# Kernel optimization log

Measured on AMD Instinct MI355X. Metric: run time of the kernel, lower is better.

The kernel has to match this reference:

```python
import jax, jax.numpy as jnp
import numpy as np
from jax import lax

B, D, BOND, OUT = 16384, 784, 5, 10

def setup_inputs() -> dict:
    key = jax.random.key(0)
    k = jax.random.split(key, 6)
    x = jax.random.uniform(k[0], (B, D), dtype=jnp.float32)
    core_first = jax.random.normal(k[1], (1, 2, BOND), dtype=jnp.float32) * 0.1
    cores_mid = jax.random.normal(k[2], (D - 2, BOND, 2, BOND), dtype=jnp.float32) * 0.1
    core_last = jax.random.normal(k[3], (BOND, 2, 1), dtype=jnp.float32) * 0.1
    # xavier_uniform for fc.weight with fan_in=1, fan_out=OUT
    bound = float(np.sqrt(6.0 / (1 + OUT)))
    fc_w = jax.random.uniform(k[4], (OUT, 1), dtype=jnp.float32, minval=-bound, maxval=bound)
    fc_b = jnp.zeros((OUT,), dtype=jnp.float32)
    return {"x": x, "core_first": core_first, "cores_mid": cores_mid,
            "core_last": core_last, "fc_w": fc_w, "fc_b": fc_b}

def reference(x, core_first, cores_mid, core_last, fc_w, fc_b):
    # x: [B, D] -> feature map [B, D, 2] = stack(1-x, x)
    xs = jnp.stack([1.0 - x, x], axis=-1)            # [B, D, 2]
    # first core: (1, 2, bond) -> initial carry [B, bond]
    carry0 = jnp.einsum('bi,ir->br', xs[:, 0], core_first[0])  # [B, bond]
    # sequential tensor-train contraction over middle sites via scan
    xs_mid = jnp.moveaxis(xs[:, 1:-1], 1, 0)          # [D-2, B, 2]
    def step(carry, inp):
        xi, core = inp                                # xi: [B,2], core: [bond,2,bond]
        carry = jnp.einsum('bl,bi,lir->br', carry, xi, core)
        return carry, None
    carry, _ = lax.scan(step, carry0, (xs_mid, cores_mid))
    # last core: (bond, 2, 1) -> scalar per batch element
    vlast = jnp.einsum('bi,li->bl', xs[:, -1], core_last[:, :, 0])  # [B, bond]
    res = jnp.sum(carry * vlast, axis=-1, keepdims=True)            # [B, 1]
    out = res @ fc_w.T + fc_b                          # [B, OUT]
    return out
```

## Files before the change

kernel.cpp:

```cpp
#include <hip/hip_runtime.h>


typedef float v4f __attribute__((ext_vector_type(4)));
typedef float v2f __attribute__((ext_vector_type(2)));

constexpr int Bn     = 16384;
constexpr int Dn     = 784;
constexpr int NOUT   = 10;
constexpr int NPAIR  = 390;
constexpr int PVEC   = 20;
constexpr int PMAT   = 25;
constexpr int RHP0   = 195;
constexpr int BWD_P0 = 370;
constexpr int PAIR_F = 100;
constexpr int WROFF  = Bn * 5;

__device__ __forceinline__ v4f splat4(float x) { v4f v = {x, x, x, x}; return v; }
__device__ __forceinline__ v4f fma4(v4f a, v4f b, v4f c) {
    return __builtin_elementwise_fma(a, b, c);
}

struct Frag { v4f r[5]; float c4[5]; };
struct CMat { v4f row[5]; v4f c4v; float c44; };

__device__ __forceinline__ void build_C(CMat& C, const float* __restrict__ s,
                                        v2f xc) {
    const float xa = xc[0], xb = xc[1], xab = xa * xb;
    const v4f va = splat4(xa), vb = splat4(xb), vp = splat4(xab);
    const v4f* s4 = (const v4f*)s;
#pragma unroll
    for (int l = 0; l < 5; ++l)
        C.row[l] = fma4(vp, s4[15 + l], fma4(vb, s4[10 + l], fma4(va, s4[5 + l], s4[l])));
#pragma unroll
    for (int l = 0; l < 4; ++l) {
        v4f cq = s4[20 + l];
        C.c4v[l] = fmaf(xab, cq[3], fmaf(xb, cq[2], fmaf(xa, cq[1], cq[0])));
    }
    {
        v4f cq = s4[24];
        C.c44 = fmaf(xab, cq[3], fmaf(xb, cq[2], fmaf(xa, cq[1], cq[0])));
    }
}

__device__ __forceinline__ void matmulIP(Frag& M, const CMat& C) {
#pragma unroll
    for (int i = 0; i < 5; ++i) {
        v4f acc  = splat4(M.r[i][0]) * C.row[0];
        float a4 = M.r[i][0] * C.c4v[0];
#pragma unroll
        for (int l = 1; l < 4; ++l) {
            acc = fma4(splat4(M.r[i][l]), C.row[l], acc);
            a4  = fmaf(M.r[i][l], C.c4v[l], a4);
        }
        acc = fma4(splat4(M.c4[i]), C.row[4], acc);
        a4  = fmaf(M.c4[i], C.c44, a4);
        M.r[i] = acc; M.c4[i] = a4;
    }
}

__device__ __forceinline__ void vecstepC(v4f& cv, float& c4, const CMat& C) {
    v4f acc  = splat4(cv[0]) * C.row[0];
    float a4 = cv[0] * C.c4v[0];
#pragma unroll
    for (int l = 1; l < 4; ++l) {
        acc = fma4(splat4(cv[l]), C.row[l], acc);
        a4  = fmaf(cv[l], C.c4v[l], a4);
    }
    acc = fma4(splat4(c4), C.row[4], acc);
    a4  = fmaf(c4, C.c44, a4);
    cv = acc; c4 = a4;
}

__global__ void prepack_pairs(const float* __restrict__ cm, float* __restrict__ pk)
{
    int idx = blockIdx.x * 256 + threadIdx.x;
    if (idx >= NPAIR * 100) return;
    int p = idx / 100, rest = idx - p * 100;
    int q = rest / 25, e = rest - q * 25;
    int l = e / 5, r = e - l * 5;
    int m1 = 2 * p + 1, m2 = 2 * p + 2;
    const float* L = cm + (size_t)(m1 * 5 + l) * 10;
    float acc = 0.f;
#pragma unroll
    for (int k = 0; k < 5; ++k) {
        float Lk = (q & 1) ? (L[5 + k] - L[k]) : L[k];
        const float* R = cm + (size_t)(m2 * 5 + k) * 10;
        float Rk = (q & 2) ? (R[5 + r] - R[r]) : R[r];
        acc = fmaf(Lk, Rk, acc);
    }
    int wl = l, wr = r;
    if (p >= BWD_P0) { wl = r; wr = l; }
    int off;
    if (wr < 4)      off = q * 20 + wl * 4 + wr;
    else if (wl < 4) off = 80 + wl * 4 + q;
    else             off = 96 + q;
    pk[(size_t)p * PAIR_F + off] = acc;
}

__global__ __launch_bounds__(512, 2)
void mps_half_kernel(const float* __restrict__ x,
                     const float* __restrict__ core_first,
                     const float* __restrict__ cores_mid,
                     const float* __restrict__ core_last,
                     const float* __restrict__ pk,
                     float* __restrict__ out)
{
    __shared__ float matbuf[4][25][128];

    const int lane = threadIdx.x & 63;
    const int wave = threadIdx.x >> 6;
    const int wu   = __builtin_amdgcn_readfirstlane(wave);
    const int g    = blockIdx.x >> 1;
    const int h    = blockIdx.x & 1;
    const int rowA = g * 128 + lane;
    const int rowB = rowA + 64;
    const v2f* __restrict__ xA2 = (const v2f*)(x + (size_t)rowA * Dn);
    const v2f* __restrict__ xB2 = (const v2f*)(x + (size_t)rowB * Dn);

    if (wu >= 1) {
        const int p0 = (h == 0 ? PVEC : RHP0) + PMAT * (wu - 1);

        Frag MA, MB;
        MA.r[0] = {1,0,0,0}; MA.r[1] = {0,1,0,0}; MA.r[2] = {0,0,1,0};
        MA.r[3] = {0,0,0,1}; MA.r[4] = {0,0,0,0};
        MA.c4[0] = 0; MA.c4[1] = 0; MA.c4[2] = 0; MA.c4[3] = 0; MA.c4[4] = 1;
        MB = MA;

        v2f xA = xA2[p0 + 1], xB = xB2[p0 + 1];
#pragma unroll 1
        for (int j = 0; j < PMAT; ++j) {
            const float* s = pk + (size_t)(p0 + j) * PAIR_F;
            v2f nxA = xA2[p0 + j + 2], nxB = xB2[p0 + j + 2];
            CMat C;
            build_C(C, s, xA);  matmulIP(MA, C);
            build_C(C, s, xB);  matmulIP(MB, C);
            xA = nxA; xB = nxB;
        }

        const int ord  = (h == 0) ? (wu - 1) : (7 - wu);
        const bool ph1 = (ord < 4);
        const int  k   = ph1 ? ord : ord - 4;
        if (ph1) {
#pragma unroll
            for (int i = 0; i < 5; ++i) {
#pragma unroll
                for (int r = 0; r < 4; ++r) {
                    matbuf[k][i * 5 + r][lane]      = MA.r[i][r];
                    matbuf[k][i * 5 + r][lane + 64] = MB.r[i][r];
                }
                matbuf[k][i * 5 + 4][lane]      = MA.c4[i];
                matbuf[k][i * 5 + 4][lane + 64] = MB.c4[i];
            }
        }
        __syncthreads();
        __syncthreads();
        if (!ph1) {
#pragma unroll
            for (int i = 0; i < 5; ++i) {
#pragma unroll
                for (int r = 0; r < 4; ++r) {
                    matbuf[k][i * 5 + r][lane]      = MA.r[i][r];
                    matbuf[k][i * 5 + r][lane + 64] = MB.r[i][r];
                }
                matbuf[k][i * 5 + 4][lane]      = MA.c4[i];
                matbuf[k][i * 5 + 4][lane + 64] = MB.c4[i];
            }
        }
        __syncthreads();
    } else if (h == 0) {
        v2f xA01 = xA2[0], xB01 = xB2[0];
        float clA[5], clB[5], cnA[5], cnB[5];
#pragma unroll
        for (int r = 0; r < 5; ++r) {
            float d = core_first[5 + r] - core_first[r];
            clA[r] = fmaf(xA01[0], d, core_first[r]);
            clB[r] = fmaf(xB01[0], d, core_first[r]);
        }
        const float* cm0 = cores_mid;
#pragma unroll
        for (int r = 0; r < 5; ++r) {
            float aA = 0.f, aB = 0.f;
#pragma unroll
            for (int l = 0; l < 5; ++l) {
                float base = cm0[l * 10 + r], d = cm0[l * 10 + 5 + r] - base;
                aA = fmaf(clA[l], fmaf(xA01[1], d, base), aA);
                aB = fmaf(clB[l], fmaf(xB01[1], d, base), aB);
            }
            cnA[r] = aA; cnB[r] = aB;
        }
        v4f cvA = {cnA[0], cnA[1], cnA[2], cnA[3]};
        v4f cvB = {cnB[0], cnB[1], cnB[2], cnB[3]};
        float c4A = cnA[4], c4B = cnB[4];

        v2f xA = xA2[1], xB = xB2[1];
#pragma unroll 1
        for (int p = 0; p < PVEC; ++p) {
            const float* s = pk + (size_t)p * PAIR_F;
            v2f nxA = xA2[p + 2], nxB = xB2[p + 2];
            CMat C;
            build_C(C, s, xA);  vecstepC(cvA, c4A, C);
            build_C(C, s, xB);  vecstepC(cvB, c4B, C);
            xA = nxA; xB = nxB;
        }
        clA[0] = cvA[0]; clA[1] = cvA[1]; clA[2] = cvA[2]; clA[3] = cvA[3]; clA[4] = c4A;
        clB[0] = cvB[0]; clB[1] = cvB[1]; clB[2] = cvB[2]; clB[3] = cvB[3]; clB[4] = c4B;

        __syncthreads();
#pragma unroll 1
        for (int k = 0; k < 4; ++k) {
            float vA[5], vB[5];
#pragma unroll
            for (int r = 0; r < 5; ++r) {
                vA[r] = clA[0] * matbuf[k][r][lane];
                vB[r] = clB[0] * matbuf[k][r][lane + 64];
            }
#pragma unroll
            for (int l = 1; l < 5; ++l)
#pragma unroll
                for (int r = 0; r < 5; ++r) {
                    vA[r] = fmaf(clA[l], matbuf[k][l * 5 + r][lane],      vA[r]);
                    vB[r] = fmaf(clB[l], matbuf[k][l * 5 + r][lane + 64], vB[r]);
                }
#pragma unroll
            for (int r = 0; r < 5; ++r) { clA[r] = vA[r]; clB[r] = vB[r]; }
        }
        __syncthreads();
        __syncthreads();
#pragma unroll 1
        for (int k = 0; k < 3; ++k) {
            float vA[5], vB[5];
#pragma unroll
            for (int r = 0; r < 5; ++r) {
                vA[r] = clA[0] * matbuf[k][r][lane];
                vB[r] = clB[0] * matbuf[k][r][lane + 64];
            }
#pragma unroll
            for (int l = 1; l < 5; ++l)
#pragma unroll
                for (int r = 0; r < 5; ++r) {
                    vA[r] = fmaf(clA[l], matbuf[k][l * 5 + r][lane],      vA[r]);
                    vB[r] = fmaf(clB[l], matbuf[k][l * 5 + r][lane + 64], vB[r]);
                }
#pragma unroll
            for (int r = 0; r < 5; ++r) { clA[r] = vA[r]; clB[r] = vB[r]; }
        }
        float* oA = out + (size_t)rowA * 5;
        float* oB = out + (size_t)rowB * 5;
#pragma unroll
        for (int i = 0; i < 5; ++i) { oA[i] = clA[i]; oB[i] = clB[i]; }
    } else {
        v2f xAz = xA2[391], xBz = xB2[391];
        float vlA[5], vlB[5], vnA[5], vnB[5];
#pragma unroll
        for (int l = 0; l < 5; ++l) {
            float base = core_last[2 * l], d = core_last[2 * l + 1] - base;
            vlA[l] = fmaf(xAz[1], d, base);
            vlB[l] = fmaf(xBz[1], d, base);
        }
        const float* cmL = cores_mid + (size_t)781 * 50;
#pragma unroll
        for (int l = 0; l < 5; ++l) {
            float aA = 0.f, aB = 0.f;
#pragma unroll
            for (int r = 0; r < 5; ++r) {
                float base = cmL[l * 10 + r], d = cmL[l * 10 + 5 + r] - base;
                aA = fmaf(fmaf(xAz[0], d, base), vlA[r], aA);
                aB = fmaf(fmaf(xBz[0], d, base), vlB[r], aB);
            }
            vnA[l] = aA; vnB[l] = aB;
        }
        v4f cvA = {vnA[0], vnA[1], vnA[2], vnA[3]};
        v4f cvB = {vnB[0], vnB[1], vnB[2], vnB[3]};
        float c4A = vnA[4], c4B = vnB[4];

        v2f xA = xA2[390], xB = xB2[390];
#pragma unroll 1
        for (int p = 389; p >= BWD_P0; --p) {
            const float* s = pk + (size_t)p * PAIR_F;
            v2f nxA = xA2[p], nxB = xB2[p];
            CMat C;
            build_C(C, s, xA);  vecstepC(cvA, c4A, C);
            build_C(C, s, xB);  vecstepC(cvB, c4B, C);
            xA = nxA; xB = nxB;
        }
        float uA[5] = {cvA[0], cvA[1], cvA[2], cvA[3], c4A};
        float uB[5] = {cvB[0], cvB[1], cvB[2], cvB[3], c4B};

        __syncthreads();
#pragma unroll 1
        for (int k = 0; k < 4; ++k) {
            float vA[5], vB[5];
#pragma unroll
            for (int i = 0; i < 5; ++i) {
                float aA = matbuf[k][i * 5][lane]      * uA[0];
                float aB = matbuf[k][i * 5][lane + 64] * uB[0];
#pragma unroll
                for (int l = 1; l < 5; ++l) {
                    aA = fmaf(matbuf[k][i * 5 + l][lane],      uA[l], aA);
                    aB = fmaf(matbuf[k][i * 5 + l][lane + 64], uB[l], aB);
                }
                vA[i] = aA; vB[i] = aB;
            }
#pragma unroll
            for (int i = 0; i < 5; ++i) { uA[i] = vA[i]; uB[i] = vB[i]; }
        }
        __syncthreads();
        __syncthreads();
#pragma unroll 1
        for (int k = 0; k < 3; ++k) {
            float vA[5], vB[5];
#pragma unroll
            for (int i = 0; i < 5; ++i) {
                float aA = matbuf[k][i * 5][lane]      * uA[0];
                float aB = matbuf[k][i * 5][lane + 64] * uB[0];
#pragma unroll
                for (int l = 1; l < 5; ++l) {
                    aA = fmaf(matbuf[k][i * 5 + l][lane],      uA[l], aA);
                    aB = fmaf(matbuf[k][i * 5 + l][lane + 64], uB[l], aB);
                }
                vA[i] = aA; vB[i] = aB;
            }
#pragma unroll
            for (int i = 0; i < 5; ++i) { uA[i] = vA[i]; uB[i] = vB[i]; }
        }
        float* oA = out + WROFF + (size_t)rowA * 5;
        float* oB = out + WROFF + (size_t)rowB * 5;
#pragma unroll
        for (int i = 0; i < 5; ++i) { oA[i] = uA[i]; oB[i] = uB[i]; }
    }
}

__global__ __launch_bounds__(256)
void finish_dot(const float* __restrict__ outF, float* __restrict__ res)
{
    int r = blockIdx.x * 256 + threadIdx.x;
    const float* vl = outF + (size_t)r * 5;
    const float* wr = outF + WROFF + (size_t)r * 5;
    float s = vl[0] * wr[0];
#pragma unroll
    for (int i = 1; i < 5; ++i) s = fmaf(vl[i], wr[i], s);
    res[r] = s;
}

__global__ __launch_bounds__(256)
void finish_out(const float* __restrict__ res, const float* __restrict__ fc_w,
                const float* __restrict__ fc_b, float* __restrict__ out)
{
    int r = blockIdx.x * 256 + threadIdx.x;
    float rv = res[r];
    float* o = out + (size_t)r * NOUT;
#pragma unroll
    for (int j = 0; j < NOUT; ++j) o[j] = fmaf(rv, fc_w[j], fc_b[j]);
}

extern "C" void kernel_launch(void* const* d_in, const int* in_sizes, int n_in,
                              void* d_out, int out_size, void* d_ws, size_t ws_size,
                              hipStream_t stream) {
    const float* x          = (const float*)d_in[0];
    const float* core_first = (const float*)d_in[1];
    const float* cores_mid  = (const float*)d_in[2];
    const float* core_last  = (const float*)d_in[3];
    const float* fc_w       = (const float*)d_in[4];
    const float* fc_b       = (const float*)d_in[5];
    float* out              = (float*)d_out;
    float* pk               = (float*)d_ws;
    float* res              = (float*)d_ws;

    hipLaunchKernelGGL(prepack_pairs, dim3((NPAIR * 100 + 255) / 256), dim3(256),
                       0, stream, cores_mid, pk);
    hipLaunchKernelGGL(mps_half_kernel, dim3(256), dim3(512), 0, stream,
                       x, core_first, cores_mid, core_last, pk, out);
    hipLaunchKernelGGL(finish_dot, dim3(Bn / 256), dim3(256), 0, stream,
                       out, res);
    hipLaunchKernelGGL(finish_out, dim3(Bn / 256), dim3(256), 0, stream,
                       res, fc_w, fc_b, out);
}
```

Measured before the change: 146.0 us.

## Split the chain into four segments per row group across 512 blocks

Adds a quarter-split kernel in which each 128-row group is handled by four blocks instead of two. Each block covers a shorter stretch of sites: the two middle segments fold their partial 5x5 transfer matrices and write them to workspace, and a new finish kernel combines them with the left and right vectors. This doubles the block count and shortens the per-wave sequential chains to expose more parallelism on the GPU. In exchange it adds global traffic for the intermediate matrices and an extra combine step. The old half-split path remains as a fallback when the workspace is too small.

```diff
diff --git a/kernel.cpp b/kernel.cpp
--- a/kernel.cpp
+++ b/kernel.cpp
@@ -8,12 +8,10 @@
 constexpr int Dn     = 784;
 constexpr int NOUT   = 10;
 constexpr int NPAIR  = 390;
-constexpr int PVEC   = 20;
-constexpr int PMAT   = 25;
-constexpr int RHP0   = 195;
-constexpr int BWD_P0 = 370;
 constexpr int PAIR_F = 100;
 constexpr int WROFF  = Bn * 5;
+constexpr int PK_F   = 40960;
+constexpr int M_OFF  = PK_F;
 
 __device__ __forceinline__ v4f splat4(float x) { v4f v = {x, x, x, x}; return v; }
 __device__ __forceinline__ v4f fma4(v4f a, v4f b, v4f c) {
@@ -71,7 +69,40 @@
     cv = acc; c4 = a4;
 }
 
-__global__ void prepack_pairs(const float* __restrict__ cm, float* __restrict__ pk)
+__device__ __forceinline__ void mat_chain(Frag& MA, Frag& MB, int p0, int n,
+                                          const float* __restrict__ pk,
+                                          const v2f* __restrict__ xA2,
+                                          const v2f* __restrict__ xB2) {
+    v2f xA = xA2[p0 + 1], xB = xB2[p0 + 1];
+#pragma unroll 1
+    for (int j = 0; j < n; ++j) {
+        const float* s = pk + (size_t)(p0 + j) * PAIR_F;
+        v2f nxA = xA2[p0 + j + 2], nxB = xB2[p0 + j + 2];
+        CMat C;
+        build_C(C, s, xA);  matmulIP(MA, C);
+        build_C(C, s, xB);  matmulIP(MB, C);
+        xA = nxA; xB = nxB;
+    }
+}
+
+__device__ __forceinline__ void foldM(Frag& M, const float (*mb)[128], int ln) {
+#pragma unroll
+    for (int i = 0; i < 5; ++i) {
+        float v[5];
+#pragma unroll
+        for (int r = 0; r < 5; ++r) {
+            float a = M.r[i][0] * mb[r][ln];
+#pragma unroll
+            for (int l = 1; l < 4; ++l) a = fmaf(M.r[i][l], mb[l * 5 + r][ln], a);
+            a = fmaf(M.c4[i], mb[20 + r][ln], a);
+            v[r] = a;
+        }
+        M.r[i] = {v[0], v[1], v[2], v[3]}; M.c4[i] = v[4];
+    }
+}
+
+__global__ void prepack_pairs(const float* __restrict__ cm, float* __restrict__ pk,
+                              int bwd0)
 {
     int idx = blockIdx.x * 256 + threadIdx.x;
     if (idx >= NPAIR * 100) return;
@@ -89,13 +120,306 @@
         acc = fmaf(Lk, Rk, acc);
     }
     int wl = l, wr = r;
-    if (p >= BWD_P0) { wl = r; wr = l; }
+    if (p >= bwd0) { wl = r; wr = l; }
     int off;
     if (wr < 4)      off = q * 20 + wl * 4 + wr;
     else if (wl < 4) off = 80 + wl * 4 + q;
     else             off = 96 + q;
     pk[(size_t)p * PAIR_F + off] = acc;
 }
+
+
+__global__ __launch_bounds__(512, 2)
+void mps_quarter_kernel(const float* __restrict__ x,
+                        const float* __restrict__ core_first,
+                        const float* __restrict__ cores_mid,
+                        const float* __restrict__ core_last,
+                        float* __restrict__ ws,
+                        float* __restrict__ out)
+{
+    __shared__ float matbuf[4][25][128];
+
+    const float* __restrict__ pk = ws;
+    const int lane = threadIdx.x & 63;
+    const int wave = threadIdx.x >> 6;
+    const int wu   = __builtin_amdgcn_readfirstlane(wave);
+    const int g    = blockIdx.x >> 2;
+    const int seg  = blockIdx.x & 3;
+    const int rowA = g * 128 + lane;
+    const int rowB = rowA + 64;
+    const v2f* __restrict__ xA2 = (const v2f*)(x + (size_t)rowA * Dn);
+    const v2f* __restrict__ xB2 = (const v2f*)(x + (size_t)rowB * Dn);
+
+    if (wu >= 1) {
+        const int m0 = (seg == 0) ? 13 : (seg == 1) ? 111 : (seg == 2) ? 209 : 293;
+        const int p0 = m0 + 12 * (wu - 1);
+
+        Frag MA, MB;
+        MA.r[0] = {1,0,0,0}; MA.r[1] = {0,1,0,0}; MA.r[2] = {0,0,1,0};
+        MA.r[3] = {0,0,0,1}; MA.r[4] = {0,0,0,0};
+        MA.c4[0] = 0; MA.c4[1] = 0; MA.c4[2] = 0; MA.c4[3] = 0; MA.c4[4] = 1;
+        MB = MA;
+
+        mat_chain(MA, MB, p0, 12, pk, xA2, xB2);
+
+        const int ord  = (seg == 3) ? (7 - wu) : (wu - 1);
+        const bool ph1 = (ord < 4);
+        const int  k   = ph1 ? ord : ord - 4;
+        if (ph1) {
+#pragma unroll
+            for (int i = 0; i < 5; ++i) {
+#pragma unroll
+                for (int r = 0; r < 4; ++r) {
+                    matbuf[k][i * 5 + r][lane]      = MA.r[i][r];
+                    matbuf[k][i * 5 + r][lane + 64] = MB.r[i][r];
+                }
+                matbuf[k][i * 5 + 4][lane]      = MA.c4[i];
+                matbuf[k][i * 5 + 4][lane + 64] = MB.c4[i];
+            }
+        }
+        __syncthreads();
+        __syncthreads();
+        if (!ph1) {
+#pragma unroll
+            for (int i = 0; i < 5; ++i) {
+#pragma unroll
+                for (int r = 0; r < 4; ++r) {
+                    matbuf[k][i * 5 + r][lane]      = MA.r[i][r];
+                    matbuf[k][i * 5 + r][lane + 64] = MB.r[i][r];
+                }
+                matbuf[k][i * 5 + 4][lane]      = MA.c4[i];
+                matbuf[k][i * 5 + 4][lane + 64] = MB.c4[i];
+            }
+        }
+        __syncthreads();
+    } else if (seg == 0) {
+        v2f xA01 = xA2[0], xB01 = xB2[0];
+        float clA[5], clB[5], cnA[5], cnB[5];
+#pragma unroll
+        for (int r = 0; r < 5; ++r) {
+            float d = core_first[5 + r] - core_first[r];
+            clA[r] = fmaf(xA01[0], d, core_first[r]);
+            clB[r] = fmaf(xB01[0], d, core_first[r]);
+        }
+        const float* cm0 = cores_mid;
+#pragma unroll
+        for (int r = 0; r < 5; ++r) {
+            float aA = 0.f, aB = 0.f;
+#pragma unroll
+            for (int l = 0; l < 5; ++l) {
+                float base = cm0[l * 10 + r], d = cm0[l * 10 + 5 + r] - base;
+                aA = fmaf(clA[l], fmaf(xA01[1], d, base), aA);
+                aB = fmaf(clB[l], fmaf(xB01[1], d, base), aB);
+            }
+            cnA[r] = aA; cnB[r] = aB;
+        }
+        v4f cvA = {cnA[0], cnA[1], cnA[2], cnA[3]};
+        v4f cvB = {cnB[0], cnB[1], cnB[2], cnB[3]};
+        float c4A = cnA[4], c4B = cnB[4];
+
+        v2f xA = xA2[1], xB = xB2[1];
+#pragma unroll 1
+        for (int p = 0; p < 13; ++p) {
+            const float* s = pk + (size_t)p * PAIR_F;
+            v2f nxA = xA2[p + 2], nxB = xB2[p + 2];
+            CMat C;
+            build_C(C, s, xA);  vecstepC(cvA, c4A, C);
+            build_C(C, s, xB);  vecstepC(cvB, c4B, C);
+            xA = nxA; xB = nxB;
+        }
+        clA[0] = cvA[0]; clA[1] = cvA[1]; clA[2] = cvA[2]; clA[3] = cvA[3]; clA[4] = c4A;
+        clB[0] = cvB[0]; clB[1] = cvB[1]; clB[2] = cvB[2]; clB[3] = cvB[3]; clB[4] = c4B;
+
+        __syncthreads();
+#pragma unroll 1
+        for (int k = 0; k < 4; ++k) {
+            float vA[5], vB[5];
+#pragma unroll
+            for (int r = 0; r < 5; ++r) {
+                vA[r] = clA[0] * matbuf[k][r][lane];
+                vB[r] = clB[0] * matbuf[k][r][lane + 64];
+            }
+#pragma unroll
+            for (int l = 1; l < 5; ++l)
+#pragma unroll
+                for (int r = 0; r < 5; ++r) {
+                    vA[r] = fmaf(clA[l], matbuf[k][l * 5 + r][lane],      vA[r]);
+                    vB[r] = fmaf(clB[l], matbuf[k][l * 5 + r][lane + 64], vB[r]);
+                }
+#pragma unroll
+            for (int r = 0; r < 5; ++r) { clA[r] = vA[r]; clB[r] = vB[r]; }
+        }
+        __syncthreads();
+        __syncthreads();
+#pragma unroll 1
+        for (int k = 0; k < 3; ++k) {
+            float vA[5], vB[5];
+#pragma unroll
+            for (int r = 0; r < 5; ++r) {
+                vA[r] = clA[0] * matbuf[k][r][lane];
+                vB[r] = clB[0] * matbuf[k][r][lane + 64];
+            }
+#pragma unroll
+            for (int l = 1; l < 5; ++l)
+#pragma unroll
+                for (int r = 0; r < 5; ++r) {
+                    vA[r] = fmaf(clA[l], matbuf[k][l * 5 + r][lane],      vA[r]);
+                    vB[r] = fmaf(clB[l], matbuf[k][l * 5 + r][lane + 64], vB[r]);
+                }
+#pragma unroll
+            for (int r = 0; r < 5; ++r) { clA[r] = vA[r]; clB[r] = vB[r]; }
+        }
+        float* oA = out + (size_t)rowA * 5;
+        float* oB = out + (size_t)rowB * 5;
+#pragma unroll
+        for (int i = 0; i < 5; ++i) { oA[i] = clA[i]; oB[i] = clB[i]; }
+    } else if (seg == 3) {
+        v2f xAz = xA2[391], xBz = xB2[391];
+        float vlA[5], vlB[5], vnA[5], vnB[5];
+#pragma unroll
+        for (int l = 0; l < 5; ++l) {
+            float base = core_last[2 * l], d = core_last[2 * l + 1] - base;
+            vlA[l] = fmaf(xAz[1], d, base);
+            vlB[l] = fmaf(xBz[1], d, base);
+        }
+        const float* cmL = cores_mid + (size_t)781 * 50;
+#pragma unroll
+        for (int l = 0; l < 5; ++l) {
+            float aA = 0.f, aB = 0.f;
+#pragma unroll
+            for (int r = 0; r < 5; ++r) {
+                float base = cmL[l * 10 + r], d = cmL[l * 10 + 5 + r] - base;
+                aA = fmaf(fmaf(xAz[0], d, base), vlA[r], aA);
+                aB = fmaf(fmaf(xBz[0], d, base), vlB[r], aB);
+            }
+            vnA[l] = aA; vnB[l] = aB;
+        }
+        v4f cvA = {vnA[0], vnA[1], vnA[2], vnA[3]};
+        v4f cvB = {vnB[0], vnB[1], vnB[2], vnB[3]};
+        float c4A = vnA[4], c4B = vnB[4];
+
+        v2f xA = xA2[390], xB = xB2[390];
+#pragma unroll 1
+        for (int p = 389; p >= 377; --p) {
+            const float* s = pk + (size_t)p * PAIR_F;
+            v2f nxA = xA2[p], nxB = xB2[p];
+            CMat C;
+            build_C(C, s, xA);  vecstepC(cvA, c4A, C);
+            build_C(C, s, xB);  vecstepC(cvB, c4B, C);
+            xA = nxA; xB = nxB;
+        }
+        float uA[5] = {cvA[0], cvA[1], cvA[2], cvA[3], c4A};
+        float uB[5] = {cvB[0], cvB[1], cvB[2], cvB[3], c4B};
+
+        __syncthreads();
+#pragma unroll 1
+        for (int k = 0; k < 4; ++k) {
+            float vA[5], vB[5];
+#pragma unroll
+            for (int i = 0; i < 5; ++i) {
+                float aA = matbuf[k][i * 5][lane]      * uA[0];
+                float aB = matbuf[k][i * 5][lane + 64] * uB[0];
+#pragma unroll
+                for (int l = 1; l < 5; ++l) {
+                    aA = fmaf(matbuf[k][i * 5 + l][lane],      uA[l], aA);
+                    aB = fmaf(matbuf[k][i * 5 + l][lane + 64], uB[l], aB);
+                }
+                vA[i] = aA; vB[i] = aB;
+            }
+#pragma unroll
+            for (int i = 0; i < 5; ++i) { uA[i] = vA[i]; uB[i] = vB[i]; }
+        }
+        __syncthreads();
+        __syncthreads();
+#pragma unroll 1
+        for (int k = 0; k < 3; ++k) {
+            float vA[5], vB[5];
+#pragma unroll
+            for (int i = 0; i < 5; ++i) {
+                float aA = matbuf[k][i * 5][lane]      * uA[0];
+                float aB = matbuf[k][i * 5][lane + 64] * uB[0];
+#pragma unroll
+                for (int l = 1; l < 5; ++l) {
+                    aA = fmaf(matbuf[k][i * 5 + l][lane],      uA[l], aA);
+                    aB = fmaf(matbuf[k][i * 5 + l][lane + 64], uB[l], aB);
+                }
+                vA[i] = aA; vB[i] = aB;
+            }
+#pragma unroll
+            for (int i = 0; i < 5; ++i) { uA[i] = vA[i]; uB[i] = vB[i]; }
+        }
+        float* oA = out + WROFF + (size_t)rowA * 5;
+        float* oB = out + WROFF + (size_t)rowB * 5;
+#pragma unroll
+        for (int i = 0; i < 5; ++i) { oA[i] = uA[i]; oB[i] = uB[i]; }
+    } else {
+        const int p0 = (seg == 1) ? 97 : 195;
+
+        Frag MA, MB;
+        MA.r[0] = {1,0,0,0}; MA.r[1] = {0,1,0,0}; MA.r[2] = {0,0,1,0};
+        MA.r[3] = {0,0,0,1}; MA.r[4] = {0,0,0,0};
+        MA.c4[0] = 0; MA.c4[1] = 0; MA.c4[2] = 0; MA.c4[3] = 0; MA.c4[4] = 1;
+        MB = MA;
+
+        mat_chain(MA, MB, p0, 14, pk, xA2, xB2);
+
+        __syncthreads();
+#pragma unroll 1
+        for (int k = 0; k < 4; ++k) {
+            foldM(MA, matbuf[k], lane);
+            foldM(MB, matbuf[k], lane + 64);
+        }
+        __syncthreads();
+        __syncthreads();
+#pragma unroll 1
+        for (int k = 0; k < 3; ++k) {
+            foldM(MA, matbuf[k], lane);
+            foldM(MB, matbuf[k], lane + 64);
+        }
+        float* mA = ws + M_OFF + ((size_t)(seg - 1) * Bn + rowA) * 25;
+        float* mB = ws + M_OFF + ((size_t)(seg - 1) * Bn + rowB) * 25;
+#pragma unroll
+        for (int i = 0; i < 5; ++i) {
+#pragma unroll
+            for (int r = 0; r < 4; ++r) {
+                mA[i * 5 + r] = MA.r[i][r];
+                mB[i * 5 + r] = MB.r[i][r];
+            }
+            mA[i * 5 + 4] = MA.c4[i];
+            mB[i * 5 + 4] = MB.c4[i];
+        }
+    }
+}
+
+__global__ __launch_bounds__(256)
+void finish_dot_q(const float* __restrict__ outF, float* __restrict__ ws)
+{
+    int row = blockIdx.x * 256 + threadIdx.x;
+    const float* vl = outF + (size_t)row * 5;
+    const float* wr = outF + WROFF + (size_t)row * 5;
+    const float* M1 = ws + M_OFF + (size_t)row * 25;
+    const float* M2 = ws + M_OFF + ((size_t)Bn + row) * 25;
+    float t[5], v[5];
+#pragma unroll
+    for (int r = 0; r < 5; ++r) {
+        float a = vl[0] * M1[r];
+#pragma unroll
+        for (int l = 1; l < 5; ++l) a = fmaf(vl[l], M1[l * 5 + r], a);
+        t[r] = a;
+    }
+#pragma unroll
+    for (int r = 0; r < 5; ++r) {
+        float a = t[0] * M2[r];
+#pragma unroll
+        for (int l = 1; l < 5; ++l) a = fmaf(t[l], M2[l * 5 + r], a);
+        v[r] = a;
+    }
+    float res = v[0] * wr[0];
+#pragma unroll
+    for (int i = 1; i < 5; ++i) res = fmaf(v[i], wr[i], res);
+    ws[row] = res;
+}
+
 
 __global__ __launch_bounds__(512, 2)
 void mps_half_kernel(const float* __restrict__ x,
@@ -118,24 +442,13 @@
     const v2f* __restrict__ xB2 = (const v2f*)(x + (size_t)rowB * Dn);
 
     if (wu >= 1) {
-        const int p0 = (h == 0 ? PVEC : RHP0) + PMAT * (wu - 1);
-
+        const int p0 = (h == 0 ? 20 : 195) + 25 * (wu - 1);
         Frag MA, MB;
         MA.r[0] = {1,0,0,0}; MA.r[1] = {0,1,0,0}; MA.r[2] = {0,0,1,0};
         MA.r[3] = {0,0,0,1}; MA.r[4] = {0,0,0,0};
         MA.c4[0] = 0; MA.c4[1] = 0; MA.c4[2] = 0; MA.c4[3] = 0; MA.c4[4] = 1;
         MB = MA;
-
-        v2f xA = xA2[p0 + 1], xB = xB2[p0 + 1];
-#pragma unroll 1
-        for (int j = 0; j < PMAT; ++j) {
-            const float* s = pk + (size_t)(p0 + j) * PAIR_F;
-            v2f nxA = xA2[p0 + j + 2], nxB = xB2[p0 + j + 2];
-            CMat C;
-            build_C(C, s, xA);  matmulIP(MA, C);
-            build_C(C, s, xB);  matmulIP(MB, C);
-            xA = nxA; xB = nxB;
-        }
+        mat_chain(MA, MB, p0, 25, pk, xA2, xB2);
 
         const int ord  = (h == 0) ? (wu - 1) : (7 - wu);
         const bool ph1 = (ord < 4);
@@ -194,7 +507,7 @@
 
         v2f xA = xA2[1], xB = xB2[1];
 #pragma unroll 1
-        for (int p = 0; p < PVEC; ++p) {
+        for (int p = 0; p < 20; ++p) {
             const float* s = pk + (size_t)p * PAIR_F;
             v2f nxA = xA2[p + 2], nxB = xB2[p + 2];
             CMat C;
@@ -275,7 +588,7 @@
 
         v2f xA = xA2[390], xB = xB2[390];
 #pragma unroll 1
-        for (int p = 389; p >= BWD_P0; --p) {
+        for (int p = 389; p >= 370; --p) {
             const float* s = pk + (size_t)p * PAIR_F;
             v2f nxA = xA2[p], nxB = xB2[p];
             CMat C;
@@ -331,7 +644,7 @@
 }
 
 __global__ __launch_bounds__(256)
-void finish_dot(const float* __restrict__ outF, float* __restrict__ res)
+void finish_dot_h(const float* __restrict__ outF, float* __restrict__ res)
 {
     int r = blockIdx.x * 256 + threadIdx.x;
     const float* vl = outF + (size_t)r * 5;
@@ -363,15 +676,27 @@
     const float* fc_w       = (const float*)d_in[4];
     const float* fc_b       = (const float*)d_in[5];
     float* out              = (float*)d_out;
-    float* pk               = (float*)d_ws;
-    float* res              = (float*)d_ws;
-
-    hipLaunchKernelGGL(prepack_pairs, dim3((NPAIR * 100 + 255) / 256), dim3(256),
-                       0, stream, cores_mid, pk);
-    hipLaunchKernelGGL(mps_half_kernel, dim3(256), dim3(512), 0, stream,
-                       x, core_first, cores_mid, core_last, pk, out);
-    hipLaunchKernelGGL(finish_dot, dim3(Bn / 256), dim3(256), 0, stream,
-                       out, res);
-    hipLaunchKernelGGL(finish_out, dim3(Bn / 256), dim3(256), 0, stream,
-                       res, fc_w, fc_b, out);
-}
+    float* ws               = (float*)d_ws;
+
+    const size_t q_need = (size_t)(M_OFF + 2 * Bn * 25) * sizeof(float);
+
+    if (ws_size >= q_need) {
+        hipLaunchKernelGGL(prepack_pairs, dim3((NPAIR * 100 + 255) / 256), dim3(256),
+                           0, stream, cores_mid, ws, 377);
+        hipLaunchKernelGGL(mps_quarter_kernel, dim3(512), dim3(512), 0, stream,
+                           x, core_first, cores_mid, core_last, ws, out);
+        hipLaunchKernelGGL(finish_dot_q, dim3(Bn / 256), dim3(256), 0, stream,
+                           out, ws);
+        hipLaunchKernelGGL(finish_out, dim3(Bn / 256), dim3(256), 0, stream,
+                           ws, fc_w, fc_b, out);
+    } else {
+        hipLaunchKernelGGL(prepack_pairs, dim3((NPAIR * 100 + 255) / 256), dim3(256),
+                           0, stream, cores_mid, ws, 370);
+        hipLaunchKernelGGL(mps_half_kernel, dim3(256), dim3(512), 0, stream,
+                           x, core_first, cores_mid, core_last, ws, out);
+        hipLaunchKernelGGL(finish_dot_h, dim3(Bn / 256), dim3(256), 0, stream,
+                           out, ws);
+        hipLaunchKernelGGL(finish_out, dim3(Bn / 256), dim3(256), 0, stream,
+                           ws, fc_w, fc_b, out);
+    }
+}
```

Result: no change. 148.5 us (+1.7%).
